# Kernel tuning notes

Hardware: AMD Instinct MI355X
Metric: run time of the kernel (lower is better)

## Reference

```python
import jax, jax.numpy as jnp
import numpy as np

# ---- constants from __init__ ----
DT = 1.0
NX, NY = 192, 192
SRC_X, SRC_Y = 40, 96
PX = jnp.array([160, 160, 160])
PY = jnp.array([48, 96, 144])
PML_N, PML_P, PML_MAX = 20, 4.0, 3.0
C0, C1 = 1.0, 0.9
H = DT * 2.01 / 1.0  # grid spacing


def make_b():
    """PML damping profile b(x,y), [NX, NY]."""
    v = (PML_MAX * np.linspace(0.0, 1.0, PML_N + 1) ** PML_P).astype(np.float32)
    bx = np.zeros((NX, NY), np.float32)
    bx[: PML_N + 1, :] = v[::-1, None]
    bx[NX - PML_N - 1 :, :] = v[:, None]
    by = np.zeros((NX, NY), np.float32)
    by[:, : PML_N + 1] = v[::-1][None, :]
    by[:, NY - PML_N - 1 :] = v[None, :]
    return jnp.asarray(np.sqrt(bx ** 2 + by ** 2))


def _conv3(img, kern):
    # img [B,1,H,W], kern [1,1,3,3], 'same' padding
    return jax.lax.conv_general_dilated(
        img, kern, (1, 1), ((1, 1), (1, 1)),
        dimension_numbers=("NCHW", "OIHW", "NCHW"))


def _proj(x, eta=0.5, beta=100.0):
    return (jnp.tanh(beta * eta) + jnp.tanh(beta * (x - eta))) / (
        jnp.tanh(beta * eta) + jnp.tanh(beta * (1.0 - eta)))


def setup_inputs() -> dict:
    key = jax.random.key(0)
    k1, k2 = jax.random.split(key)
    x = jax.random.normal(k1, (4, 256), dtype=jnp.float32)  # [batch, T]
    rho = jax.random.uniform(k2, (NX, NY), dtype=jnp.float32)
    # clip_pml_rho(): rho[b != 0] = 0 for binarized model (applied at init)
    rho = jnp.where(make_b() != 0, 0.0, rho)
    return {"x": x, "rho": rho}


def reference(x, rho):
    b = make_b()
    lpf_k = jnp.array([[[[0.0, 0.125, 0.0], [0.125, 0.5, 0.125], [0.0, 0.125, 0.0]]]], jnp.float32)
    lap_k = (H ** -2) * jnp.array([[[[0.0, 1.0, 0.0], [1.0, -4.0, 1.0], [0.0, 1.0, 0.0]]]], jnp.float32)
    A1 = 1.0 / (DT ** -2 + b * 0.5 / DT)
    A2 = 2.0 * DT ** -2
    A3 = DT ** -2 - b * 0.5 / DT

    # binarized wave-speed field c(rho): LPF then tanh projection
    lpf_rho = _conv3(rho[None, None], lpf_k)[0, 0]
    c = C0 + (C1 - C0) * _proj(lpf_rho)
    c2 = c * c

    B = x.shape[0]
    y0 = jnp.zeros((B, NX, NY), x.dtype)

    def step(carry, xi):
        y1, y2 = carry
        lap = _conv3(y1[:, None], lap_k)[:, 0]            # [B,NX,NY]
        y = A1 * (A2 * y1 - A3 * y2 + c2 * lap)
        y = y.at[:, SRC_X, SRC_Y].add(xi)                 # source injection
        return (y, y1), y[:, PX, PY]                      # emit probe values [B,P]

    _, probes = jax.lax.scan(step, (y0, y0), x.T)         # probes [T,B,P]

    # integrate_probe_points: sum |y|^2 over time, normalize per batch
    I = jnp.sum(probes ** 2, axis=0)                      # [B,P]
    return I / jnp.sum(I, axis=1, keepdims=True)
```

## Files before the change

kernel.cpp:

```cpp
#include <hip/hip_runtime.h>
#include <math.h>

#define NXY    192
#define CELLS  (NXY*NXY)
#define NBATCH 4
#define NSTEPS 256
#define TCH    16
#define NCHUNK (NSTEPS/TCH)
#define TPB    512
#define NW     8
#define RPL    5
#define OUTR   6
#define NBLKS  256

#define I_OFF   (16*CELLS)
#define FLG_OFF (I_OFF + 64)

typedef float v2f __attribute__((ext_vector_type(2)));

__device__ __forceinline__ float dpp_up1(float v) {
    int r = __builtin_amdgcn_update_dpp(0, __builtin_bit_cast(int, v),
                                        0x138, 0xf, 0xf, true);
    return __builtin_bit_cast(float, r);
}
__device__ __forceinline__ float dpp_dn1(float v) {
    int r = __builtin_amdgcn_update_dpp(0, __builtin_bit_cast(int, v),
                                        0x130, 0xf, 0xf, true);
    return __builtin_bit_cast(float, r);
}

__device__ __forceinline__ float pml_prof(int i) {
    int t;
    if (i <= 20)            t = 20 - i;
    else if (i >= NXY - 21) t = i - (NXY - 21);
    else                    return 0.0f;
    float u  = (float)t * 0.05f;
    float u2 = u * u;
    return 3.0f * u2 * u2;
}

__global__ __launch_bounds__(TPB, 1)
void wave_k(const float* __restrict__ x, const float* __restrict__ rho,
            float* __restrict__ ws, float* __restrict__ out) {
    int blk = ((blockIdx.x & 7) << 5) | (blockIdx.x >> 3);
    int b  = blk / 64;
    int r_ = blk % 64;
    int bi = r_ >> 1, cj = r_ & 1;
    int I0 = OUTR * bi - 17;
    int J0 = 96 * cj - 16;
    int t  = threadIdx.x;
    int w  = t >> 6;
    int l  = t & 63;
    int row0 = I0 + RPL * w;
    int gj   = J0 + 2 * l;

    int* flags = (int*)(ws + FLG_OFF);
    int drt = bi + (t >> 1) - 3;
    int dfi = b * 64 + drt * 2 + (t & 1);
    bool dvalid = (t < 14) && (drt >= 0) && (drt < 32);

    __shared__ v2f hb[2][2][NW + 2][64];
    __shared__ float xs[NSTEPS];
    for (int k = t; k < 2 * 2 * (NW + 2) * 64; k += TPB)
        ((v2f*)hb)[k] = (v2f){0.f, 0.f};
    if (t < NSTEPS) xs[t] = x[b * NSTEPS + t];

    bool cok = (gj >= 0 && gj < NXY);

    v2f Ka[RPL], Qa[RPL];
    {
        v2f rv[RPL + 2];
#pragma unroll
        for (int r = 0; r < RPL + 2; r++) {
            int gi = row0 - 1 + r;
            bool ok = cok && gi >= 0 && gi < NXY;
            rv[r] = ok ? *(const v2f*)(rho + gi * NXY + gj) : (v2f){0.f, 0.f};
        }
        const float IH2 = (float)(1.0 / (2.01 * 2.01));
#pragma unroll
        for (int r = 0; r < RPL; r++) {
            int gi = row0 + r;
            v2f rc = rv[r + 1], ru = rv[r], rd = rv[r + 2];
            float lf = dpp_up1(rc.y);
            float rt = dpp_dn1(rc.x);
            float bx = pml_prof(gi);
            v2f K, Q;
            {
                float lpf = 0.5f * rc.x + 0.125f * ((ru.x + rd.x) + (lf + rc.y));
                float p   = 0.5f * (1.0f + tanhf(100.0f * (lpf - 0.5f)));
                float c   = 1.0f - 0.1f * p;
                float by  = pml_prof(gj);
                float bb  = sqrtf(bx * bx + by * by);
                float a1  = 1.0f / (1.0f + 0.5f * bb);
                K.x = a1 * (c * c * IH2);
                Q.x = 1.0f - 2.0f * a1;
            }
            {
                float lpf = 0.5f * rc.y + 0.125f * ((ru.y + rd.y) + (rc.x + rt));
                float p   = 0.5f * (1.0f + tanhf(100.0f * (lpf - 0.5f)));
                float c   = 1.0f - 0.1f * p;
                float by  = pml_prof(gj + 1);
                float bb  = sqrtf(bx * bx + by * by);
                float a1  = 1.0f / (1.0f + 0.5f * bb);
                K.y = a1 * (c * c * IH2);
                Q.y = 1.0f - 2.0f * a1;
            }
            bool ok = cok && gi >= 0 && gi < NXY;
            Ka[r] = ok ? K : (v2f){0.f, 0.f};
            Qa[r] = ok ? Q : (v2f){0.f, 0.f};
        }
    }

    v2f yc[RPL], yp[RPL];
#pragma unroll
    for (int r = 0; r < RPL; r++) { yc[r] = (v2f){0.f, 0.f}; yp[r] = (v2f){0.f, 0.f}; }

    int sr = 40 - I0, sc = 96 - J0;
    bool wave_src = (sr >= RPL * w) && (sr < RPL * w + RPL);
    int src_rl = sr - RPL * w;
    float srcm = (2 * l == sc) ? 1.f : 0.f;

    int pcl = 2 * l + J0;
    bool wave_prb = (bi == 26) && (w == 4);
    const int prb_rl = 1;
    bool is_prb = (cj == 0) ? (pcl == 48) : (pcl == 96 || pcl == 144);
    float prbm = is_prb ? 1.f : 0.f;
    float pacc = 0.f;

    v2f uph, dnh;
    __syncthreads();

#define ROWC(CUR, PRV, rr_, UP, DN, XSV, YN) do {                              \
    v2f cv = CUR[rr_];                                                         \
    float lf0 = dpp_up1(cv.y);                                                 \
    float rt1 = dpp_dn1(cv.x);                                                 \
    v2f h = (v2f){lf0, rt1} + __builtin_shufflevector(cv, cv, 1, 0);           \
    v2f S = ((UP) + (DN)) + h;                                                 \
    YN = cv + Qa[rr_] * (PRV[rr_] - cv) + Ka[rr_] * (S - 4.0f * cv);           \
    if (wave_src && (rr_) == src_rl) YN.x += srcm * (XSV);                     \
    if (wave_prb && (rr_) == prb_rl) { float q = prbm * YN.x; pacc += q * YN.x; } \
} while (0)

#define STEP(CUR, PRV, PH, SIDX) do {                                          \
    v2f t0, t4;                                                                \
    ROWC(CUR, PRV, 0, uph,    CUR[1], xv[SIDX], t0);                           \
    ROWC(CUR, PRV, 4, CUR[3], dnh,    xv[SIDX], t4);                           \
    hb[PH][0][w + 1][l] = t0;                                                  \
    hb[PH][1][w + 1][l] = t4;                                                  \
    PRV[0] = t0; PRV[4] = t4;                                                  \
    _Pragma("unroll")                                                          \
    for (int r = 1; r <= 3; r++) {                                             \
        v2f y;                                                                 \
        ROWC(CUR, PRV, r, CUR[r - 1], CUR[r + 1], xv[SIDX], y);                \
        PRV[r] = y;                                                            \
    }                                                                          \
    __syncthreads();                                                           \
    uph = hb[PH][1][w][l];                                                     \
    dnh = hb[PH][0][w + 2][l];                                                 \
} while (0)

#pragma unroll 1
    for (int chunk = 0; chunk < NCHUNK; chunk++) {
        float xv[TCH];
#pragma unroll
        for (int i = 0; i < TCH; i++) xv[i] = xs[chunk * TCH + i];

        if (chunk) {
            if (dvalid) {
                while (__hip_atomic_load(&flags[dfi], __ATOMIC_RELAXED,
                                         __HIP_MEMORY_SCOPE_AGENT) < chunk) {}
            }
            __syncthreads();

            int pin = chunk & 1;
            const float* curg = ws + ((pin * 2 + 0) * NBATCH + b) * CELLS;
            const float* prvg = ws + ((pin * 2 + 1) * NBATCH + b) * CELLS;
            int  idxr[RPL];
            bool okr[RPL];
#pragma unroll
            for (int r = 0; r < RPL; r++) {
                int gi = row0 + r;
                okr[r]  = cok && gi >= 0 && gi < NXY;
                idxr[r] = okr[r] ? gi * NXY + gj : 0;
            }
            v2f c0, c1, c2, c3, c4, p0, p1, p2, p3, p4;
            asm volatile(
                "global_load_dwordx2 %0, %10, off sc0 sc1\n\t"
                "global_load_dwordx2 %1, %11, off sc0 sc1\n\t"
                "global_load_dwordx2 %2, %12, off sc0 sc1\n\t"
                "global_load_dwordx2 %3, %13, off sc0 sc1\n\t"
                "global_load_dwordx2 %4, %14, off sc0 sc1\n\t"
                "global_load_dwordx2 %5, %15, off sc0 sc1\n\t"
                "global_load_dwordx2 %6, %16, off sc0 sc1\n\t"
                "global_load_dwordx2 %7, %17, off sc0 sc1\n\t"
                "global_load_dwordx2 %8, %18, off sc0 sc1\n\t"
                "global_load_dwordx2 %9, %19, off sc0 sc1\n\t"
                "s_waitcnt vmcnt(0)"
                : "=&v"(c0), "=&v"(c1), "=&v"(c2), "=&v"(c3), "=&v"(c4),
                  "=&v"(p0), "=&v"(p1), "=&v"(p2), "=&v"(p3), "=&v"(p4)
                : "v"(curg + idxr[0]), "v"(curg + idxr[1]), "v"(curg + idxr[2]),
                  "v"(curg + idxr[3]), "v"(curg + idxr[4]),
                  "v"(prvg + idxr[0]), "v"(prvg + idxr[1]), "v"(prvg + idxr[2]),
                  "v"(prvg + idxr[3]), "v"(prvg + idxr[4])
                : "memory");
            yc[0] = okr[0] ? c0 : (v2f){0.f, 0.f};
            yc[1] = okr[1] ? c1 : (v2f){0.f, 0.f};
            yc[2] = okr[2] ? c2 : (v2f){0.f, 0.f};
            yc[3] = okr[3] ? c3 : (v2f){0.f, 0.f};
            yc[4] = okr[4] ? c4 : (v2f){0.f, 0.f};
            yp[0] = okr[0] ? p0 : (v2f){0.f, 0.f};
            yp[1] = okr[1] ? p1 : (v2f){0.f, 0.f};
            yp[2] = okr[2] ? p2 : (v2f){0.f, 0.f};
            yp[3] = okr[3] ? p3 : (v2f){0.f, 0.f};
            yp[4] = okr[4] ? p4 : (v2f){0.f, 0.f};
        }

        hb[0][0][w + 1][l] = yc[0];
        hb[0][1][w + 1][l] = yc[4];
        __syncthreads();
        uph = hb[0][1][w][l];
        dnh = hb[0][0][w + 2][l];

#pragma unroll
        for (int s2 = 0; s2 < TCH / 2; s2++) {
            STEP(yc, yp, 1, 2 * s2);
            STEP(yp, yc, 0, 2 * s2 + 1);
        }

        if (chunk != NCHUNK - 1) {
            int pout = (chunk & 1) ^ 1;
            float* ncurg = ws + ((pout * 2 + 0) * NBATCH + b) * CELLS;
            float* nprvg = ws + ((pout * 2 + 1) * NBATCH + b) * CELLS;
#pragma unroll
            for (int r = 0; r < RPL; r++) {
                int gi = row0 + r;
                if (gi >= OUTR * bi && gi < OUTR * bi + OUTR && l >= 8 && l < 56) {
                    int idx = gi * NXY + gj;
                    asm volatile(
                        "global_store_dwordx2 %0, %2, off sc0 sc1\n\t"
                        "global_store_dwordx2 %1, %3, off sc0 sc1"
                        :: "v"(ncurg + idx), "v"(nprvg + idx),
                           "v"(yc[r]), "v"(yp[r])
                        : "memory");
                }
            }
        } else {
            if (wave_prb && is_prb) {
                float* ip = ws + I_OFF + b * 3 + (pcl / 48 - 1);
                asm volatile("global_store_dword %0, %1, off sc0 sc1"
                             :: "v"(ip), "v"(pacc) : "memory");
            }
        }

        asm volatile("s_waitcnt vmcnt(0)" ::: "memory");
        __syncthreads();
        if (t == 0) {
            __hip_atomic_store(&flags[blk], chunk + 1, __ATOMIC_RELAXED,
                               __HIP_MEMORY_SCOPE_AGENT);
        }
    }
#undef STEP
#undef ROWC

    if (blk == 0) {
        if (t < 8) {
            int pb = (t >> 1) * 64 + 52 + (t & 1);
            while (__hip_atomic_load(&flags[pb], __ATOMIC_RELAXED,
                                     __HIP_MEMORY_SCOPE_AGENT) < NCHUNK) {}
        }
        __syncthreads();
        if (t < 12) {
            const float* I = ws + I_OFF;
            int bb = t / 3;
            float s = 0.f;
#pragma unroll
            for (int k = 0; k < 3; k++)
                s += __hip_atomic_load(I + 3 * bb + k, __ATOMIC_RELAXED,
                                       __HIP_MEMORY_SCOPE_AGENT);
            float num = __hip_atomic_load(I + t, __ATOMIC_RELAXED,
                                          __HIP_MEMORY_SCOPE_AGENT);
            out[t] = num / s;
        }
    }
}

extern "C" void kernel_launch(void* const* d_in, const int* in_sizes, int n_in,
                              void* d_out, int out_size, void* d_ws, size_t ws_size,
                              hipStream_t stream) {
    const float* x   = (const float*)d_in[0];
    const float* rho = (const float*)d_in[1];
    float* ws  = (float*)d_ws;
    float* outp = (float*)d_out;

    hipMemsetAsync((char*)d_ws + I_OFF * sizeof(float), 0,
                   (64 + NBLKS) * sizeof(float), stream);

    void* args[] = {(void*)&x, (void*)&rho, (void*)&ws, (void*)&outp};
    hipLaunchCooperativeKernel(wave_k, dim3(NBLKS), dim3(TPB), args, 0, stream);
}
```

Before: 215.1 us.

## Split per-block ready flags by writer wave and drop end-of-chunk block barrier

Only waves 3 and 4, which own the output rows, now write the halo exchange. Each of those waves publishes its own flag (flagsA or flagsB) once its stores drain, replacing the block-wide waitcnt, __syncthreads and single-thread flag store at the end of every chunk. Consumers wait on both flag arrays from the neighbour blocks and skip their own block, and the launch changes from a cooperative launch to a plain launch. This cuts the per-chunk synchronisation latency. It relies on all 256 blocks being co-resident without a cooperative-launch guarantee, and on other waves not overwriting the shared halo buffer early without the removed barrier.

```diff
diff --git a/kernel.cpp b/kernel.cpp
--- a/kernel.cpp
+++ b/kernel.cpp
@@ -54,10 +54,16 @@
     int row0 = I0 + RPL * w;
     int gj   = J0 + 2 * l;
 
-    int* flags = (int*)(ws + FLG_OFF);
-    int drt = bi + (t >> 1) - 3;
-    int dfi = b * 64 + drt * 2 + (t & 1);
-    bool dvalid = (t < 14) && (drt >= 0) && (drt < 32);
+    int* flagsA = (int*)(ws + FLG_OFF);
+    int* flagsB = flagsA + NBLKS;
+    int di   = t % 14;
+    int arr  = t / 14;
+    int drt  = bi + (di >> 1) - 3;
+    int dcol = di & 1;
+    int dfi  = b * 64 + drt * 2 + dcol;
+    bool dvalid = (t < 28) && (drt >= 0) && (drt < 32) &&
+                  !(drt == bi && dcol == cj);
+    const int* dflag = (arr ? flagsB : flagsA) + dfi;
 
     __shared__ v2f hb[2][2][NW + 2][64];
     __shared__ float xs[NSTEPS];
@@ -167,7 +173,7 @@
 
         if (chunk) {
             if (dvalid) {
-                while (__hip_atomic_load(&flags[dfi], __ATOMIC_RELAXED,
+                while (__hip_atomic_load(dflag, __ATOMIC_RELAXED,
                                          __HIP_MEMORY_SCOPE_AGENT) < chunk) {}
             }
             __syncthreads();
@@ -227,36 +233,37 @@
             STEP(yp, yc, 0, 2 * s2 + 1);
         }
 
-        if (chunk != NCHUNK - 1) {
-            int pout = (chunk & 1) ^ 1;
-            float* ncurg = ws + ((pout * 2 + 0) * NBATCH + b) * CELLS;
-            float* nprvg = ws + ((pout * 2 + 1) * NBATCH + b) * CELLS;
-#pragma unroll
-            for (int r = 0; r < RPL; r++) {
-                int gi = row0 + r;
-                if (gi >= OUTR * bi && gi < OUTR * bi + OUTR && l >= 8 && l < 56) {
-                    int idx = gi * NXY + gj;
-                    asm volatile(
-                        "global_store_dwordx2 %0, %2, off sc0 sc1\n\t"
-                        "global_store_dwordx2 %1, %3, off sc0 sc1"
-                        :: "v"(ncurg + idx), "v"(nprvg + idx),
-                           "v"(yc[r]), "v"(yp[r])
-                        : "memory");
+        if (w == 3 || w == 4) {
+            if (chunk != NCHUNK - 1) {
+                int pout = (chunk & 1) ^ 1;
+                float* ncurg = ws + ((pout * 2 + 0) * NBATCH + b) * CELLS;
+                float* nprvg = ws + ((pout * 2 + 1) * NBATCH + b) * CELLS;
+#pragma unroll
+                for (int r = 0; r < RPL; r++) {
+                    int gi = row0 + r;
+                    if (gi >= OUTR * bi && gi < OUTR * bi + OUTR && l >= 8 && l < 56) {
+                        int idx = gi * NXY + gj;
+                        asm volatile(
+                            "global_store_dwordx2 %0, %2, off sc0 sc1\n\t"
+                            "global_store_dwordx2 %1, %3, off sc0 sc1"
+                            :: "v"(ncurg + idx), "v"(nprvg + idx),
+                               "v"(yc[r]), "v"(yp[r])
+                            : "memory");
+                    }
                 }
-            }
-        } else {
-            if (wave_prb && is_prb) {
-                float* ip = ws + I_OFF + b * 3 + (pcl / 48 - 1);
-                asm volatile("global_store_dword %0, %1, off sc0 sc1"
-                             :: "v"(ip), "v"(pacc) : "memory");
-            }
-        }
-
-        asm volatile("s_waitcnt vmcnt(0)" ::: "memory");
-        __syncthreads();
-        if (t == 0) {
-            __hip_atomic_store(&flags[blk], chunk + 1, __ATOMIC_RELAXED,
-                               __HIP_MEMORY_SCOPE_AGENT);
+            } else {
+                if (wave_prb && is_prb) {
+                    float* ip = ws + I_OFF + b * 3 + (pcl / 48 - 1);
+                    asm volatile("global_store_dword %0, %1, off sc0 sc1"
+                                 :: "v"(ip), "v"(pacc) : "memory");
+                }
+            }
+            asm volatile("s_waitcnt vmcnt(0)" ::: "memory");
+            if (l == 0) {
+                int* f = (w == 3 ? flagsA : flagsB) + blk;
+                __hip_atomic_store(f, chunk + 1, __ATOMIC_RELAXED,
+                                   __HIP_MEMORY_SCOPE_AGENT);
+            }
         }
     }
 #undef STEP
@@ -265,7 +272,7 @@
     if (blk == 0) {
         if (t < 8) {
             int pb = (t >> 1) * 64 + 52 + (t & 1);
-            while (__hip_atomic_load(&flags[pb], __ATOMIC_RELAXED,
+            while (__hip_atomic_load(&flagsB[pb], __ATOMIC_RELAXED,
                                      __HIP_MEMORY_SCOPE_AGENT) < NCHUNK) {}
         }
         __syncthreads();
@@ -293,8 +300,7 @@
     float* outp = (float*)d_out;
 
     hipMemsetAsync((char*)d_ws + I_OFF * sizeof(float), 0,
-                   (64 + NBLKS) * sizeof(float), stream);
-
-    void* args[] = {(void*)&x, (void*)&rho, (void*)&ws, (void*)&outp};
-    hipLaunchCooperativeKernel(wave_k, dim3(NBLKS), dim3(TPB), args, 0, stream);
-}
+                   (64 + 2 * NBLKS) * sizeof(float), stream);
+
+    wave_k<<<dim3(NBLKS), dim3(TPB), 0, stream>>>(x, rho, ws, outp);
+}
```

Measured after the change: 194.3 us. 9.7% less time.
